# Kernel tuning notes

Hardware: AMD Instinct MI355X
Metric: run time of the kernel (lower is better)

Reference implementation:

```python
import jax, jax.numpy as jnp
import numpy as np

B, CIN, H, W = 4, 256, 56, 56
COUT, K = 256, 3
STRIDE, PAD, OG = 1, 1, 1
KK = K * K


def setup_inputs() -> dict:
    key = jax.random.key(0)
    k1, k2, k3, k4 = jax.random.split(key, 4)
    x = jax.random.normal(k1, (B, CIN, H, W), jnp.float32)
    # deformable conv weight [Cout, Cin/groups, K, K]
    weight = jax.random.normal(k2, (COUT, CIN, K, K), jnp.float32) * 0.05
    # offset-predicting 3x3 conv: 2*OG*K*K output channels (small init -> modest offsets)
    off_w = jax.random.normal(k3, (2 * OG * KK, CIN, 3, 3), jnp.float32) * 0.01
    off_b = jax.random.normal(k4, (2 * OG * KK,), jnp.float32) * 0.01
    return {"x": x, "weight": weight, "off_w": off_w, "off_b": off_b}


def _deform_conv(x, weight, off_w, off_b):
    Bn, C, Hh, Ww = x.shape
    # offset = param_generator(x): 3x3 conv, stride 1, pad 1
    offset = jax.lax.conv_general_dilated(
        x, off_w, window_strides=(1, 1), padding=((1, 1), (1, 1)),
        dimension_numbers=("NCHW", "OIHW", "NCHW")) + off_b[None, :, None, None]
    Ho = (Hh + 2 * PAD - K) // STRIDE + 1
    Wo = (Ww + 2 * PAD - K) // STRIDE + 1
    # torchvision layout: [B, OG, KK, (dy,dx), Ho, Wo]
    off = offset.reshape(Bn, OG, KK, 2, Ho, Wo)

    kh = jnp.arange(KK) // K
    kw = jnp.arange(KK) % K
    base_y = (jnp.arange(Ho) * STRIDE - PAD)[None, :, None] + kh[:, None, None]  # [KK,Ho,1]
    base_x = (jnp.arange(Wo) * STRIDE - PAD)[None, None, :] + kw[:, None, None]  # [KK,1,Wo]
    py = base_y[None, None].astype(x.dtype) + off[:, :, :, 0]  # [B,OG,KK,Ho,Wo]
    px = base_x[None, None].astype(x.dtype) + off[:, :, :, 1]

    Cg = C // OG
    xg = x.reshape(Bn, OG, Cg, Hh * Ww)

    def gather(yc, xc, wgt):
        # zero-padded bilinear corner: out-of-bounds samples contribute 0
        valid = (yc >= 0) & (yc < Hh) & (xc >= 0) & (xc < Ww)
        idx = (jnp.clip(yc, 0, Hh - 1) * Ww + jnp.clip(xc, 0, Ww - 1)).reshape(Bn, OG, 1, -1)
        v = jnp.take_along_axis(xg, idx, axis=3)            # [B,OG,Cg,KK*Ho*Wo]
        w = (wgt * valid.astype(wgt.dtype)).reshape(Bn, OG, 1, -1)
        return v * w

    y0 = jnp.floor(py).astype(jnp.int32)
    x0 = jnp.floor(px).astype(jnp.int32)
    ty = py - y0
    tx = px - x0
    sampled = (gather(y0,     x0,     (1 - ty) * (1 - tx))
             + gather(y0,     x0 + 1, (1 - ty) * tx)
             + gather(y0 + 1, x0,     ty * (1 - tx))
             + gather(y0 + 1, x0 + 1, ty * tx))
    sampled = sampled.reshape(Bn, C, KK, Ho, Wo)
    # weighted accumulation: implicit GEMM over (Cin, KK)
    return jnp.einsum("bikhw,oik->bohw", sampled, weight.reshape(COUT, C, KK))


def reference(x, weight, off_w, off_b):
    return _deform_conv(x, weight, off_w, off_b)
```

## Files before the change

### kernel.cpp

```cpp
#include <hip/hip_runtime.h>
#include <hip/hip_bf16.h>

#define B_N   4
#define CIN_  256
#define HH_   56
#define WW_   56
#define COUT_ 256
#define KK_   9
#define HW_   3136
#define KDIM  2304
#define NOFF  (B_N*18*HW_)
#define NOUT  (B_N*COUT_*HW_)

typedef __attribute__((ext_vector_type(8))) short short8;
typedef __attribute__((ext_vector_type(4))) float float4v;

__device__ __forceinline__ short f2bf_bits(float v) {
    union { __hip_bfloat16 h; short s; } u;
    u.h = __float2bfloat16(v);
    return u.s;
}
__device__ __forceinline__ float bfbits2f(short s) {
    union { unsigned u; float f; } u2;
    u2.u = ((unsigned)(unsigned short)s) << 16;
    return u2.f;
}

#define NB_AT  2304
#define NB_XT  784
#define NB_OW3 288
__global__ __launch_bounds__(256) void k_front(const float* __restrict__ x,
                                               const float* __restrict__ wgt,
                                               const float* __restrict__ ow,
                                               short* __restrict__ At2,
                                               short* __restrict__ xTb,
                                               short* __restrict__ owT3) {
    __shared__ float tile[64][65];
    int bx = blockIdx.x;
    int t = threadIdx.x;
    if (bx < NB_AT) {
        int i = bx*256 + t;
        int e = i & 7;
        int l = (i >> 3) & 63;
        int gg = i >> 9;
        int g  = gg % 72;
        int rt = gg / 72;
        int m = rt*16 + (l & 15);
        int k = g*32 + (l >> 4)*8 + e;
        int kk = k >> 8;  int ci = k & 255;
        At2[i] = f2bf_bits(wgt[(size_t)(m*CIN_ + ci)*9 + kk]);
        return;
    }
    if (bx < NB_AT + NB_XT) {
        int g = bx - NB_AT;
        int b = g / 196; int r = g % 196;
        int c0 = (r / 49) * 64; int p0 = (r % 49) * 64;
        int tp = t & 63;  int tc = t >> 6;
        #pragma unroll
        for (int i = 0; i < 16; ++i) {
            int ci = tc*16 + i;
            tile[ci][tp] = x[((size_t)b*CIN_ + c0 + ci)*HW_ + p0 + tp];
        }
        __syncthreads();
        #pragma unroll
        for (int i = 0; i < 16; ++i) {
            int p = tc*16 + i;
            xTb[((size_t)b*HW_ + p0 + p)*CIN_ + c0 + tp] = f2bf_bits(tile[tp][p]);
        }
        return;
    }
    {
        int i = (bx - NB_AT - NB_XT)*256 + t;
        int c = i / KDIM; int r = i % KDIM;
        int kk = r >> 8;  int ci = r & 255;
        owT3[i] = (c < 18) ? f2bf_bits(ow[(size_t)(c*CIN_ + ci)*9 + kk]) : 0;
    }
}

__global__ __launch_bounds__(256) void k_offgemm(const short* __restrict__ owT3,
                                                 const short* __restrict__ xTb,
                                                 float* __restrict__ pOff2) {
    __shared__ short sA[32*64];
    __shared__ short sB[64*64];
    __shared__ int   sP2[64];
    int t = threadIdx.x;
    int posb = blockIdx.x * 64;
    int b    = blockIdx.y;
    int ks   = blockIdx.z;
    int kt0  = ks * 256;
    int kend = kt0 + 256;

    if (t < 64) {
        int pos = posb + t;
        int h = pos / WW_, w = pos % WW_;
        int yy = h + ks/3 - 1, xx = w + ks%3 - 1;
        bool v = (yy >= 0) && (yy < HH_) && (xx >= 0) && (xx < WW_);
        sP2[t] = v ? (yy*WW_ + xx) : -1;
    }
    __syncthreads();

    int arow = t >> 3,  aq  = t & 7;
    int brow = t >> 2,  bqc = (t & 3) * 2;

    int wv = t >> 6;
    int wm = (wv >> 1) * 16;
    int wn = (wv & 1) * 32;
    int lane = t & 63;
    int lm = lane & 15;
    int qd = lane >> 4;

    float4v acc[2];
    acc[0] = (float4v)(0.f); acc[1] = (float4v)(0.f);

    const short* gA = owT3 + (size_t)arow*KDIM + aq*8;
    const short* xb = xTb + (size_t)b*HW_*CIN_;

    short* wA = sA + (((arow >> 4)*8 + aq)*16 + ((arow + 2*aq) & 15))*8;
    short* wB[2];
    #pragma unroll
    for (int j = 0; j < 2; ++j) {
        int qq = bqc + j;
        wB[j] = sB + (((brow >> 4)*8 + qq)*16 + ((brow + 2*qq) & 15))*8;
    }

    short8 pa, pb[2];
    const short8 zero8 = (short8)(0);
    int p2 = sP2[brow];
    pa = *(const short8*)(gA + kt0);
    #pragma unroll
    for (int j = 0; j < 2; ++j) {
        int ci0 = (bqc + j)*8;
        pb[j] = (p2 >= 0) ? *(const short8*)(xb + (size_t)p2*CIN_ + ci0) : zero8;
    }

    for (int kt = kt0; kt < kend; kt += 64) {
        __syncthreads();
        *(short8*)wA = pa;
        #pragma unroll
        for (int j = 0; j < 2; ++j) *(short8*)wB[j] = pb[j];
        __syncthreads();
        int kt2 = kt + 64;
        if (kt2 < kend) {
            pa = *(const short8*)(gA + kt2);
            int cb = kt2 & 255;
            #pragma unroll
            for (int j = 0; j < 2; ++j) {
                int ci0 = cb + (bqc + j)*8;
                pb[j] = (p2 >= 0) ? *(const short8*)(xb + (size_t)p2*CIN_ + ci0) : zero8;
            }
        }
        #pragma unroll
        for (int kss = 0; kss < 2; ++kss) {
            int qe = kss*4 + qd;
            int sw = (lm + 2*qe) & 15;
            short8 af, bf[2];
            af = *(short8*)(sA + ((((wm>>4))*8 + qe)*16 + sw)*8);
            #pragma unroll
            for (int j = 0; j < 2; ++j)
                bf[j] = *(short8*)(sB + ((((wn>>4) + j)*8 + qe)*16 + sw)*8);
            #pragma unroll
            for (int j = 0; j < 2; ++j)
                acc[j] = __builtin_amdgcn_mfma_f32_16x16x32_bf16(
                             af, bf[j], acc[j], 0, 0, 0);
        }
    }

    float* pbase = pOff2 + (size_t)ks*NOFF;
    #pragma unroll
    for (int j = 0; j < 2; ++j) {
        int col = posb + wn + j*16 + lm;
        #pragma unroll
        for (int r = 0; r < 4; ++r) {
            int c = wm + qd*4 + r;
            if (c < 18)
                pbase[((size_t)(b*18 + c))*HW_ + col] = acc[j][r];
        }
    }
}

__global__ __launch_bounds__(512) void k_gemm(const short* __restrict__ At2,
                                              const short* __restrict__ xTb,
                                              const float* __restrict__ pOff2,
                                              const float* __restrict__ ob,
                                              float* __restrict__ pout) {
    __shared__ short sB[32*64];
    __shared__ int4   sPI[3*32];
    __shared__ float4 sPW[3*32];
    int t = threadIdx.x;

    int idx = blockIdx.x;
    int xcd = idx & 7;
    int b   = xcd & 3;
    int q   = (idx >> 3)*2 + (xcd >> 2);
    int sidx = q % 98;
    int ks   = q / 98;
    int posb = sidx * 32;

    for (int e = t; e < 3*32; e += 512) {
        int kk = ks*3 + (e >> 5); int pl = e & 31;
        int pos = posb + pl;
        int h = pos / WW_, w = pos % WW_;
        size_t oy = (size_t)(b*18 + 2*kk    )*HW_ + pos;
        size_t ox = (size_t)(b*18 + 2*kk + 1)*HW_ + pos;
        float dy = ob[2*kk], dx = ob[2*kk + 1];
        #pragma unroll
        for (int s = 0; s < 9; ++s) {
            dy += pOff2[(size_t)s*NOFF + oy];
            dx += pOff2[(size_t)s*NOFF + ox];
        }
        float py = (float)(h - 1 + kk/3) + dy;
        float px = (float)(w - 1 + kk%3) + dx;
        float y0f = floorf(py), x0f = floorf(px);
        int y0 = (int)y0f, x0 = (int)x0f;
        float ty = py - y0f, tx = px - x0f;
        bool vy0 = (y0   >= 0) && (y0   < HH_);
        bool vy1 = (y0+1 >= 0) && (y0+1 < HH_);
        bool vx0 = (x0   >= 0) && (x0   < WW_);
        bool vx1 = (x0+1 >= 0) && (x0+1 < WW_);
        int y0c = min(max(y0,   0), HH_-1), y1c = min(max(y0+1, 0), HH_-1);
        int x0c = min(max(x0,   0), WW_-1), x1c = min(max(x0+1, 0), WW_-1);
        sPI[e] = make_int4(y0c*WW_+x0c, y0c*WW_+x1c, y1c*WW_+x0c, y1c*WW_+x1c);
        sPW[e] = make_float4((vy0 && vx0) ? (1.f-ty)*(1.f-tx) : 0.f,
                             (vy0 && vx1) ? (1.f-ty)*tx       : 0.f,
                             (vy1 && vx0) ? ty*(1.f-tx)       : 0.f,
                             (vy1 && vx1) ? ty*tx             : 0.f);
    }
    __syncthreads();

    bool doB = (t < 256);
    int brow = (t & 255) >> 3;
    int bq   = t & 7;

    int wv = t >> 6;
    int lane = t & 63;
    int lm = lane & 15;
    int qd = lane >> 4;

    float4v acc[2][2];
    #pragma unroll
    for (int i = 0; i < 2; ++i)
        #pragma unroll
        for (int j = 0; j < 2; ++j) acc[i][j] = (float4v)(0.f);

    const short* xb = xTb + (size_t)b*HW_*CIN_;
    const short* pA = At2 + (((size_t)(wv*2) * 72) << 9) + (size_t)lane * 8;
    int g0 = ks * 24;

    short* wB = sB + (((brow >> 4)*8 + bq)*16 + ((brow + 2*bq) & 15))*8;

    short8 cg[4];
    float4 bwv;

#define CGLOAD(itX) do {                                                      \
    int4 id_ = sPI[((itX) >> 2)*32 + brow];                                   \
    bwv = sPW[((itX) >> 2)*32 + brow];                                        \
    int ci0_ = ((itX) & 3) * 64 + bq*8;                                       \
    cg[0] = *(const short8*)(xb + (size_t)id_.x*CIN_ + ci0_);                 \
    cg[1] = *(const short8*)(xb + (size_t)id_.y*CIN_ + ci0_);                 \
    cg[2] = *(const short8*)(xb + (size_t)id_.z*CIN_ + ci0_);                 \
    cg[3] = *(const short8*)(xb + (size_t)id_.w*CIN_ + ci0_);                 \
} while (0)

    if (doB) CGLOAD(0);

    for (int it = 0; it < 12; ++it) {
        short8 af[4];
        #pragma unroll
        for (int kss = 0; kss < 2; ++kss)
            #pragma unroll
            for (int i = 0; i < 2; ++i)
                af[kss*2 + i] = *(const short8*)(
                    pA + ((size_t)(i*72 + g0 + it*2 + kss) << 9));

        short8 pk;
        if (doB) {
            float f[8];
            #pragma unroll
            for (int e = 0; e < 8; ++e)
                f[e] = bwv.x*bfbits2f(cg[0][e]) + bwv.y*bfbits2f(cg[1][e])
                     + bwv.z*bfbits2f(cg[2][e]) + bwv.w*bfbits2f(cg[3][e]);
            union { short8 s8; __hip_bfloat162 h2[4]; } pu;
            #pragma unroll
            for (int e2 = 0; e2 < 4; ++e2)
                pu.h2[e2] = __float22bfloat162_rn(make_float2(f[2*e2], f[2*e2+1]));
            pk = pu.s8;
            if (it + 1 < 12) CGLOAD(it + 1);
        }

        __syncthreads();
        if (doB) *(short8*)wB = pk;
        __syncthreads();

        #pragma unroll
        for (int kss = 0; kss < 2; ++kss) {
            int qe = kss*4 + qd;
            int sw = (lm + 2*qe) & 15;
            short8 bf[2];
            #pragma unroll
            for (int j = 0; j < 2; ++j)
                bf[j] = *(short8*)(sB + ((j*8 + qe)*16 + sw)*8);
            #pragma unroll
            for (int i = 0; i < 2; ++i)
                #pragma unroll
                for (int j = 0; j < 2; ++j)
                    acc[i][j] = __builtin_amdgcn_mfma_f32_16x16x32_bf16(
                                    af[kss*2 + i], bf[j], acc[i][j], 0, 0, 0);
        }
    }
#undef CGLOAD

    float* pbase = pout + (size_t)ks*NOUT;
    #pragma unroll
    for (int i = 0; i < 2; ++i)
        #pragma unroll
        for (int j = 0; j < 2; ++j) {
            int col = posb + j*16 + lm;
            #pragma unroll
            for (int r = 0; r < 4; ++r) {
                int m = wv*32 + i*16 + qd*4 + r;
                pbase[((size_t)b*COUT_ + m)*HW_ + col] = acc[i][j][r];
            }
        }
}

__global__ __launch_bounds__(256) void k_oreduce(const float* __restrict__ pout,
                                                 float* __restrict__ out) {
    int i = blockIdx.x*256 + threadIdx.x;
    if (i >= NOUT/4) return;
    float4 a = ((const float4*)pout)[i];
    float4 b = ((const float4*)(pout + NOUT))[i];
    float4 c = ((const float4*)(pout + 2*(size_t)NOUT))[i];
    float4 r;
    r.x = a.x + b.x + c.x;  r.y = a.y + b.y + c.y;
    r.z = a.z + b.z + c.z;  r.w = a.w + b.w + c.w;
    ((float4*)out)[i] = r;
}

extern "C" void kernel_launch(void* const* d_in, const int* in_sizes, int n_in,
                              void* d_out, int out_size, void* d_ws, size_t ws_size,
                              hipStream_t stream) {
    const float* x   = (const float*)d_in[0];
    const float* wgt = (const float*)d_in[1];
    const float* ow  = (const float*)d_in[2];
    const float* ob  = (const float*)d_in[3];
    float* out = (float*)d_out;

    char* ws = (char*)d_ws;
    short* At2   = (short*)ws;
    short* xTb   = (short*)(ws + 1179648);
    short* owT3  = (short*)(ws + 7602176);
    float* pOff2 = (float*)(ws + 7749632);
    float* pout  = (float*)(ws + 15878144);

    k_front  <<<dim3(NB_AT + NB_XT + NB_OW3), 256, 0, stream>>>(x, wgt, ow, At2, xTb, owT3);
    k_offgemm<<<dim3(49, 4, 9),               256, 0, stream>>>(owT3, xTb, pOff2);
    k_gemm   <<<dim3(1176),                   512, 0, stream>>>(At2, xTb, pOff2, ob, pout);
    k_oreduce<<<dim3(NOUT/4/256),             256, 0, stream>>>(pout, out);
}
```

Before: 122.4 us.

## Replace split-K main GEMM with M-split over output channels, drop reduce kernel

The main deformable GEMM no longer splits the K dimension three ways with partial outputs and a separate reduction kernel. Each block now covers the full K range (36 iterations over all 9 taps) for half of the output channels, writing straight to the output, so the fp32 partial-sum round trip and one launch disappear. In exchange, the bilinear gather and interpolation of the B tile is now computed twice (once per M half), and the grid shrinks from 1176 to 784 blocks of 256 threads, each with a longer serial loop. The XCD-aware block remapping is removed as well.

```diff
diff --git a/kernel.cpp b/kernel.cpp
--- a/kernel.cpp
+++ b/kernel.cpp
@@ -94,7 +94,7 @@
         int pos = posb + t;
         int h = pos / WW_, w = pos % WW_;
         int yy = h + ks/3 - 1, xx = w + ks%3 - 1;
-        bool v = (yy >= 0) && (yy < HH_) && (xx >= 0) && (xx < WW_);
+        bool v = (yy >= 0) && (yy < HH_) && (xx < WW_) && (xx >= 0);
         sP2[t] = v ? (yy*WW_ + xx) : -1;
     }
     __syncthreads();
@@ -178,26 +178,22 @@
     }
 }
 
-__global__ __launch_bounds__(512) void k_gemm(const short* __restrict__ At2,
+__global__ __launch_bounds__(256) void k_gemm(const short* __restrict__ At2,
                                               const short* __restrict__ xTb,
                                               const float* __restrict__ pOff2,
                                               const float* __restrict__ ob,
-                                              float* __restrict__ pout) {
+                                              float* __restrict__ out) {
     __shared__ short sB[32*64];
-    __shared__ int4   sPI[3*32];
-    __shared__ float4 sPW[3*32];
+    __shared__ int4   sPI[9*32];
+    __shared__ float4 sPW[9*32];
     int t = threadIdx.x;
 
-    int idx = blockIdx.x;
-    int xcd = idx & 7;
-    int b   = xcd & 3;
-    int q   = (idx >> 3)*2 + (xcd >> 2);
-    int sidx = q % 98;
-    int ks   = q / 98;
-    int posb = sidx * 32;
-
-    for (int e = t; e < 3*32; e += 512) {
-        int kk = ks*3 + (e >> 5); int pl = e & 31;
+    int posb = blockIdx.x * 32;
+    int b    = blockIdx.y;
+    int m0   = blockIdx.z * 128;
+
+    for (int e = t; e < 9*32; e += 256) {
+        int kk = e >> 5; int pl = e & 31;
         int pos = posb + pl;
         int h = pos / WW_, w = pos % WW_;
         size_t oy = (size_t)(b*18 + 2*kk    )*HW_ + pos;
@@ -227,8 +223,7 @@
     }
     __syncthreads();
 
-    bool doB = (t < 256);
-    int brow = (t & 255) >> 3;
+    int brow = t >> 3;
     int bq   = t & 7;
 
     int wv = t >> 6;
@@ -243,8 +238,8 @@
         for (int j = 0; j < 2; ++j) acc[i][j] = (float4v)(0.f);
 
     const short* xb = xTb + (size_t)b*HW_*CIN_;
-    const short* pA = At2 + (((size_t)(wv*2) * 72) << 9) + (size_t)lane * 8;
-    int g0 = ks * 24;
+    const short* pA = At2 + (((size_t)((m0 >> 4) + wv*2) * 72) << 9)
+                          + (size_t)lane * 8;
 
     short* wB = sB + (((brow >> 4)*8 + bq)*16 + ((brow + 2*bq) & 15))*8;
 
@@ -261,19 +256,19 @@
     cg[3] = *(const short8*)(xb + (size_t)id_.w*CIN_ + ci0_);                 \
 } while (0)
 
-    if (doB) CGLOAD(0);
-
-    for (int it = 0; it < 12; ++it) {
+    CGLOAD(0);
+
+    for (int it = 0; it < 36; ++it) {
         short8 af[4];
         #pragma unroll
         for (int kss = 0; kss < 2; ++kss)
             #pragma unroll
             for (int i = 0; i < 2; ++i)
                 af[kss*2 + i] = *(const short8*)(
-                    pA + ((size_t)(i*72 + g0 + it*2 + kss) << 9));
+                    pA + ((size_t)(i*72 + it*2 + kss) << 9));
 
         short8 pk;
-        if (doB) {
+        {
             float f[8];
             #pragma unroll
             for (int e = 0; e < 8; ++e)
@@ -284,11 +279,11 @@
             for (int e2 = 0; e2 < 4; ++e2)
                 pu.h2[e2] = __float22bfloat162_rn(make_float2(f[2*e2], f[2*e2+1]));
             pk = pu.s8;
-            if (it + 1 < 12) CGLOAD(it + 1);
-        }
-
-        __syncthreads();
-        if (doB) *(short8*)wB = pk;
+        }
+        if (it + 1 < 36) CGLOAD(it + 1);
+
+        __syncthreads();
+        *(short8*)wB = pk;
         __syncthreads();
 
         #pragma unroll
@@ -309,7 +304,6 @@
     }
 #undef CGLOAD
 
-    float* pbase = pout + (size_t)ks*NOUT;
     #pragma unroll
     for (int i = 0; i < 2; ++i)
         #pragma unroll
@@ -317,23 +311,10 @@
             int col = posb + j*16 + lm;
             #pragma unroll
             for (int r = 0; r < 4; ++r) {
-                int m = wv*32 + i*16 + qd*4 + r;
-                pbase[((size_t)b*COUT_ + m)*HW_ + col] = acc[i][j][r];
+                int m = m0 + wv*32 + i*16 + qd*4 + r;
+                out[((size_t)b*COUT_ + m)*HW_ + col] = acc[i][j][r];
             }
         }
-}
-
-__global__ __launch_bounds__(256) void k_oreduce(const float* __restrict__ pout,
-                                                 float* __restrict__ out) {
-    int i = blockIdx.x*256 + threadIdx.x;
-    if (i >= NOUT/4) return;
-    float4 a = ((const float4*)pout)[i];
-    float4 b = ((const float4*)(pout + NOUT))[i];
-    float4 c = ((const float4*)(pout + 2*(size_t)NOUT))[i];
-    float4 r;
-    r.x = a.x + b.x + c.x;  r.y = a.y + b.y + c.y;
-    r.z = a.z + b.z + c.z;  r.w = a.w + b.w + c.w;
-    ((float4*)out)[i] = r;
 }
 
 extern "C" void kernel_launch(void* const* d_in, const int* in_sizes, int n_in,
@@ -350,10 +331,8 @@
     short* xTb   = (short*)(ws + 1179648);
     short* owT3  = (short*)(ws + 7602176);
     float* pOff2 = (float*)(ws + 7749632);
-    float* pout  = (float*)(ws + 15878144);
 
     k_front  <<<dim3(NB_AT + NB_XT + NB_OW3), 256, 0, stream>>>(x, wgt, ow, At2, xTb, owT3);
     k_offgemm<<<dim3(49, 4, 9),               256, 0, stream>>>(owT3, xTb, pOff2);
-    k_gemm   <<<dim3(1176),                   512, 0, stream>>>(At2, xTb, pOff2, ob, pout);
-    k_oreduce<<<dim3(NOUT/4/256),             256, 0, stream>>>(pout, out);
-}
+    k_gemm   <<<dim3(98, 4, 2),               256, 0, stream>>>(At2, xTb, pOff2, ob, out);
+}
```

Measured after the change: 128.2 us. +4.8%, slower.
